# Kernel optimization log

Measured on AMD Instinct MI355X. Metric: run time of the kernel, lower is better.

## Reference

```python
import jax, jax.numpy as jnp
import numpy as np
import math

B, T, D = 2, 2048, 2048
N_HEADS, N_KV_HEADS = 16, 4
HEAD_DIM = D // N_HEADS          # 128
N_GROUPS = N_HEADS // N_KV_HEADS # 4


def setup_inputs() -> dict:
    key = jax.random.key(0)
    k1, k2, k3, k4, k5 = jax.random.split(key, 5)
    x = jax.random.normal(k1, (B, T, D), dtype=jnp.float32)
    # RoPE table: [T, head_dim//2, 2] = (cos, sin)
    inv_freq = 1.0 / (10000.0 ** (np.arange(0, HEAD_DIM, 2, dtype=np.float32) / HEAD_DIM))
    ang = np.arange(T, dtype=np.float32)[:, None] * inv_freq[None, :]  # [T, hd/2]
    rope = jnp.asarray(np.stack([np.cos(ang), np.sin(ang)], axis=-1), dtype=jnp.float32)
    s = 0.02
    wq = s * jax.random.normal(k2, (N_HEADS * HEAD_DIM, D), dtype=jnp.float32)
    wk = s * jax.random.normal(k3, (N_KV_HEADS * HEAD_DIM, D), dtype=jnp.float32)
    wv = s * jax.random.normal(k4, (N_KV_HEADS * HEAD_DIM, D), dtype=jnp.float32)
    wo = s * jax.random.normal(k5, (D, D), dtype=jnp.float32)
    return {"x": x, "rope": rope, "wq": wq, "wk": wk, "wv": wv, "wo": wo}


def apply_rope(t, rope):
    # t: [B, H, T, hd]; rope: [T, hd/2, 2]
    d = t.shape[-1]
    t1, t2 = t[..., : d // 2], t[..., d // 2 :]
    cos = rope[..., 0][None, None]  # [1,1,T,hd/2]
    sin = rope[..., 1][None, None]
    return jnp.concatenate([t1 * cos - t2 * sin, t1 * sin + t2 * cos], axis=-1)


def reference(x, rope, wq, wk, wv, wo):
    b, t, c = x.shape
    q = (x @ wq.T).reshape(b, t, N_HEADS, HEAD_DIM).transpose(0, 2, 1, 3)
    k = (x @ wk.T).reshape(b, t, N_KV_HEADS, HEAD_DIM).transpose(0, 2, 1, 3)
    v = (x @ wv.T).reshape(b, t, N_KV_HEADS, HEAD_DIM).transpose(0, 2, 1, 3)
    q = apply_rope(q, rope)
    k = apply_rope(k, rope)
    k = jnp.repeat(k, N_GROUPS, axis=1)  # [B, H, T, hd]
    v = jnp.repeat(v, N_GROUPS, axis=1)
    scale = 1.0 / math.sqrt(HEAD_DIM)
    scores = jnp.einsum("bhqd,bhkd->bhqk", q, k) * scale
    causal = jnp.tril(jnp.ones((t, t), dtype=bool))
    scores = jnp.where(causal[None, None], scores, jnp.finfo(scores.dtype).min)
    attn = jax.nn.softmax(scores, axis=-1)
    y = jnp.einsum("bhqk,bhkd->bhqd", attn, v)
    y = y.transpose(0, 2, 1, 3).reshape(b, t, c)
    return y @ wo.T
```

## Files before the change

### kernel.cpp

```cpp
#include <hip/hip_runtime.h>

typedef unsigned short u16;
typedef float   f32x4  __attribute__((ext_vector_type(4)));
typedef short   short8 __attribute__((ext_vector_type(8)));
typedef __bf16  bf16x8 __attribute__((ext_vector_type(8)));
typedef float   float4v __attribute__((ext_vector_type(4)));
typedef unsigned short u16x4 __attribute__((ext_vector_type(4)));

static __device__ __forceinline__ u16 f2b(float f) {
  return __builtin_bit_cast(u16, (__bf16)f);
}
static __device__ __forceinline__ float b2f(u16 h) {
  union { unsigned u; float f; } v; v.u = ((unsigned)h) << 16;
  return v.f;
}
static __device__ __forceinline__ f32x4 mfma_bf16(short8 a, short8 b, f32x4 c) {
  return __builtin_amdgcn_mfma_f32_16x16x32_bf16(
      __builtin_bit_cast(bf16x8, a), __builtin_bit_cast(bf16x8, b), c, 0, 0, 0);
}
static __device__ __forceinline__ void gload_lds16(const u16* g, u16* l) {
  __builtin_amdgcn_global_load_lds(
      (const __attribute__((address_space(1))) unsigned int*)g,
      (__attribute__((address_space(3))) unsigned int*)l, 16, 0, 0);
}

#define BB 2
#define TT 2048
#define DD 2048
#define NH 16
#define NKVH 4
#define HD 128
#define MM (BB * TT)
#define QSTR 3072
#define QSCALE 0.08838834764831845f

#define N4_X   ((MM * DD) / 4)
#define N4_WQ  ((DD * DD) / 4)
#define N4_WKV ((NKVH * HD * DD) / 4)
#define N4_WO  ((DD * DD) / 4)
#define N4_TOT (N4_X + N4_WQ + 2 * N4_WKV + N4_WO)

__global__ __launch_bounds__(256) void cvt_all(const float* __restrict__ x,
                                               const float* __restrict__ wq,
                                               const float* __restrict__ wk,
                                               const float* __restrict__ wv,
                                               const float* __restrict__ wo,
                                               u16* __restrict__ xb,
                                               u16* __restrict__ wqkvb,
                                               u16* __restrict__ wob) {
  int stride = gridDim.x * blockDim.x;
  for (int i = blockIdx.x * blockDim.x + threadIdx.x; i < N4_TOT; i += stride) {
    const float4v* src;
    u16x4* dst;
    int off;
    if (i < N4_X) {
      src = (const float4v*)x; dst = (u16x4*)xb; off = i;
    } else if (i < N4_X + N4_WQ) {
      src = (const float4v*)wq; dst = (u16x4*)wqkvb; off = i - N4_X;
    } else if (i < N4_X + N4_WQ + N4_WKV) {
      src = (const float4v*)wk; dst = (u16x4*)wqkvb + N4_WQ; off = i - (N4_X + N4_WQ);
    } else if (i < N4_X + N4_WQ + 2 * N4_WKV) {
      src = (const float4v*)wv; dst = (u16x4*)wqkvb + N4_WQ + N4_WKV;
      off = i - (N4_X + N4_WQ + N4_WKV);
    } else {
      src = (const float4v*)wo; dst = (u16x4*)wob; off = i - (N4_X + N4_WQ + 2 * N4_WKV);
    }
    float4v v = src[off];
    u16x4 o;
    o[0] = f2b(v[0]); o[1] = f2b(v[1]); o[2] = f2b(v[2]); o[3] = f2b(v[3]);
    dst[off] = o;
  }
}

__global__ __launch_bounds__(256) void rope_k(u16* __restrict__ K,
                                              const float* __restrict__ rope) {
  int idx = blockIdx.x * 256 + threadIdx.x;
  int i  = idx & 63;
  int h  = (idx >> 6) & (NKVH - 1);
  int bt = idx >> 8;
  int t  = bt & (TT - 1);
  size_t base = (size_t)bt * QSTR + h * HD + i;
  float x1 = b2f(K[base]);
  float x2 = b2f(K[base + 64]);
  float c = rope[t * 128 + 2 * i];
  float s = rope[t * 128 + 2 * i + 1];
  K[base]      = f2b(x1 * c - x2 * s);
  K[base + 64] = f2b(x1 * s + x2 * c);
}

__global__ __launch_bounds__(512, 2) void gemm_qkv(const u16* __restrict__ A,
                                                   const u16* __restrict__ W,
                                                   u16* __restrict__ C,
                                                   int M, int N, int K) {
  __shared__ __align__(16) u16 As[2][2][128 * 64];
  __shared__ __align__(16) u16 Ws[2][2][128 * 64];

  const int tid = threadIdx.x, lane = tid & 63, wid = tid >> 6;
  const int wm = wid >> 2, wn = wid & 3;
  const int l15 = lane & 15, lh = lane >> 4;

  const int nwg = gridDim.x * gridDim.y;
  const int lin = blockIdx.y * gridDim.x + blockIdx.x;
  const int swz = (lin & 7) * (nwg >> 3) + (lin >> 3);
  const int brow = (swz / gridDim.x) * 256, bcol = (swz % gridDim.x) * 256;

  const int srp = wid * 8 + (lane >> 3);
  const int gsw = ((lane & 7) ^ (lane >> 3)) << 3;
  const u16* sa[2][2];
  const u16* sw[2][2];
#pragma unroll
  for (int mh = 0; mh < 2; ++mh)
#pragma unroll
    for (int i = 0; i < 2; ++i) {
      sa[mh][i] = A + (size_t)(brow + mh * 128 + i * 64 + srp) * K + gsw;
      sw[mh][i] = W + (size_t)(bcol + mh * 128 + i * 64 + srp) * K + gsw;
    }

  f32x4 acc[8][4];
#pragma unroll
  for (int mi = 0; mi < 8; ++mi)
#pragma unroll
    for (int ni = 0; ni < 4; ++ni) acc[mi][ni] = (f32x4)0.0f;

  const int nk = K >> 6;

  auto issue = [&](int t, int p) {
#pragma unroll
    for (int mh = 0; mh < 2; ++mh)
#pragma unroll
      for (int i = 0; i < 2; ++i) {
        gload_lds16(sa[mh][i] + t * 64, &As[p][mh][i * 4096 + wid * 512]);
        gload_lds16(sw[mh][i] + t * 64, &Ws[p][mh][i * 4096 + wid * 512]);
      }
  };

  issue(0, 0);
  for (int t = 0; t < nk; ++t) {
    const int p = t & 1;
    if (t + 1 < nk) {
      issue(t + 1, p ^ 1);
      asm volatile("s_waitcnt vmcnt(8)" ::: "memory");
    } else {
      asm volatile("s_waitcnt vmcnt(0)" ::: "memory");
    }
    __builtin_amdgcn_sched_barrier(0);
    __builtin_amdgcn_s_barrier();
    __builtin_amdgcn_sched_barrier(0);

    const u16* Ab = &As[p][wm][0];
    const u16* Wb = &Ws[p][wn >> 1][0];
    const int wrow = (wn & 1) * 64;

    short8 af[4][2], bf[2][2];
#pragma unroll
    for (int mi = 0; mi < 4; ++mi)
#pragma unroll
      for (int ks = 0; ks < 2; ++ks) {
        int rh = mi * 16 + l15;
        af[mi][ks] = *(const short8*)&Ab[rh * 64 + (((ks * 4 + lh) ^ (rh & 7)) << 3)];
      }
#pragma unroll
    for (int ni = 0; ni < 2; ++ni)
#pragma unroll
      for (int ks = 0; ks < 2; ++ks) {
        int rh = wrow + ni * 16 + l15;
        bf[ni][ks] = *(const short8*)&Wb[rh * 64 + (((ks * 4 + lh) ^ (rh & 7)) << 3)];
      }
    __builtin_amdgcn_s_setprio(1);
#pragma unroll
    for (int mi = 0; mi < 4; ++mi)
#pragma unroll
      for (int ni = 0; ni < 2; ++ni)
#pragma unroll
        for (int ks = 0; ks < 2; ++ks)
          acc[mi][ni] = mfma_bf16(af[mi][ks], bf[ni][ks], acc[mi][ni]);
    __builtin_amdgcn_s_setprio(0);
    __builtin_amdgcn_s_barrier();
#pragma unroll
    for (int ni = 0; ni < 2; ++ni)
#pragma unroll
      for (int ks = 0; ks < 2; ++ks) {
        int rh = wrow + (2 + ni) * 16 + l15;
        bf[ni][ks] = *(const short8*)&Wb[rh * 64 + (((ks * 4 + lh) ^ (rh & 7)) << 3)];
      }
    __builtin_amdgcn_s_setprio(1);
#pragma unroll
    for (int mi = 0; mi < 4; ++mi)
#pragma unroll
      for (int ni = 0; ni < 2; ++ni)
#pragma unroll
        for (int ks = 0; ks < 2; ++ks)
          acc[mi][2 + ni] = mfma_bf16(af[mi][ks], bf[ni][ks], acc[mi][2 + ni]);
    __builtin_amdgcn_s_setprio(0);
    __builtin_amdgcn_s_barrier();
#pragma unroll
    for (int mi = 0; mi < 4; ++mi)
#pragma unroll
      for (int ks = 0; ks < 2; ++ks) {
        int rh = (4 + mi) * 16 + l15;
        af[mi][ks] = *(const short8*)&Ab[rh * 64 + (((ks * 4 + lh) ^ (rh & 7)) << 3)];
      }
    __builtin_amdgcn_s_setprio(1);
#pragma unroll
    for (int mi = 0; mi < 4; ++mi)
#pragma unroll
      for (int ni = 0; ni < 2; ++ni)
#pragma unroll
        for (int ks = 0; ks < 2; ++ks)
          acc[4 + mi][2 + ni] = mfma_bf16(af[mi][ks], bf[ni][ks], acc[4 + mi][2 + ni]);
    __builtin_amdgcn_s_setprio(0);
    __builtin_amdgcn_s_barrier();
#pragma unroll
    for (int ni = 0; ni < 2; ++ni)
#pragma unroll
      for (int ks = 0; ks < 2; ++ks) {
        int rh = wrow + ni * 16 + l15;
        bf[ni][ks] = *(const short8*)&Wb[rh * 64 + (((ks * 4 + lh) ^ (rh & 7)) << 3)];
      }
    __builtin_amdgcn_s_setprio(1);
#pragma unroll
    for (int mi = 0; mi < 4; ++mi)
#pragma unroll
      for (int ni = 0; ni < 2; ++ni)
#pragma unroll
        for (int ks = 0; ks < 2; ++ks)
          acc[4 + mi][ni] = mfma_bf16(af[mi][ks], bf[ni][ks], acc[4 + mi][ni]);
    __builtin_amdgcn_s_setprio(0);

    asm volatile("s_waitcnt lgkmcnt(0)" ::: "memory");
    __builtin_amdgcn_sched_barrier(0);
    __builtin_amdgcn_s_barrier();
    __builtin_amdgcn_sched_barrier(0);
  }

#pragma unroll
  for (int mi = 0; mi < 8; ++mi)
#pragma unroll
    for (int ni = 0; ni < 4; ++ni)
#pragma unroll
      for (int j = 0; j < 4; ++j) {
        int row = brow + wm * 128 + mi * 16 + lh * 4 + j;
        int col = bcol + wn * 64 + ni * 16 + l15;
        C[(size_t)row * N + col] = f2b(acc[mi][ni][j]);
      }
}

__global__ __launch_bounds__(512, 2) void gemm_wo(const u16* __restrict__ A,
                                                  const u16* __restrict__ W,
                                                  float* __restrict__ C,
                                                  int M, int N, int K) {
  __shared__ __align__(16) u16 As[2][2][128 * 64];
  __shared__ __align__(16) u16 Ws[2][128 * 64];

  const int tid = threadIdx.x, lane = tid & 63, wid = tid >> 6;
  const int wm = wid >> 2, wn = wid & 3;
  const int l15 = lane & 15, lh = lane >> 4;

  const int nwg = gridDim.x * gridDim.y;
  const int lin = blockIdx.y * gridDim.x + blockIdx.x;
  const int swz = (lin & 7) * (nwg >> 3) + (lin >> 3);
  const int brow = (swz / gridDim.x) * 256, bcol = (swz % gridDim.x) * 128;

  const int srp = wid * 8 + (lane >> 3);
  const int gsw = ((lane & 7) ^ (lane >> 3)) << 3;
  const u16* sa[2][2];
  const u16* sw2[2];
#pragma unroll
  for (int mh = 0; mh < 2; ++mh)
#pragma unroll
    for (int i = 0; i < 2; ++i)
      sa[mh][i] = A + (size_t)(brow + mh * 128 + i * 64 + srp) * K + gsw;
#pragma unroll
  for (int i = 0; i < 2; ++i)
    sw2[i] = W + (size_t)(bcol + i * 64 + srp) * K + gsw;

  f32x4 acc[8][2];
#pragma unroll
  for (int mi = 0; mi < 8; ++mi)
#pragma unroll
    for (int ni = 0; ni < 2; ++ni) acc[mi][ni] = (f32x4)0.0f;

  const int nk = K >> 6;

  auto issue = [&](int t, int p) {
#pragma unroll
    for (int mh = 0; mh < 2; ++mh)
#pragma unroll
      for (int i = 0; i < 2; ++i)
        gload_lds16(sa[mh][i] + t * 64, &As[p][mh][i * 4096 + wid * 512]);
#pragma unroll
    for (int i = 0; i < 2; ++i)
      gload_lds16(sw2[i] + t * 64, &Ws[p][i * 4096 + wid * 512]);
  };

  issue(0, 0);
  for (int t = 0; t < nk; ++t) {
    const int p = t & 1;
    if (t + 1 < nk) {
      issue(t + 1, p ^ 1);
      asm volatile("s_waitcnt vmcnt(6)" ::: "memory");
    } else {
      asm volatile("s_waitcnt vmcnt(0)" ::: "memory");
    }
    __builtin_amdgcn_sched_barrier(0);
    __builtin_amdgcn_s_barrier();
    __builtin_amdgcn_sched_barrier(0);

    const u16* Ab = &As[p][wm][0];
    const u16* Wb = &Ws[p][0];

    short8 af[4][2], bf[2][2];
#pragma unroll
    for (int ni = 0; ni < 2; ++ni)
#pragma unroll
      for (int ks = 0; ks < 2; ++ks) {
        int rh = wn * 32 + ni * 16 + l15;
        bf[ni][ks] = *(const short8*)&Wb[rh * 64 + (((ks * 4 + lh) ^ (rh & 7)) << 3)];
      }
#pragma unroll
    for (int mi = 0; mi < 4; ++mi)
#pragma unroll
      for (int ks = 0; ks < 2; ++ks) {
        int rh = mi * 16 + l15;
        af[mi][ks] = *(const short8*)&Ab[rh * 64 + (((ks * 4 + lh) ^ (rh & 7)) << 3)];
      }
    __builtin_amdgcn_s_setprio(1);
#pragma unroll
    for (int mi = 0; mi < 4; ++mi)
#pragma unroll
      for (int ni = 0; ni < 2; ++ni)
#pragma unroll
        for (int ks = 0; ks < 2; ++ks)
          acc[mi][ni] = mfma_bf16(af[mi][ks], bf[ni][ks], acc[mi][ni]);
    __builtin_amdgcn_s_setprio(0);
    __builtin_amdgcn_s_barrier();
#pragma unroll
    for (int mi = 0; mi < 4; ++mi)
#pragma unroll
      for (int ks = 0; ks < 2; ++ks) {
        int rh = (4 + mi) * 16 + l15;
        af[mi][ks] = *(const short8*)&Ab[rh * 64 + (((ks * 4 + lh) ^ (rh & 7)) << 3)];
      }
    __builtin_amdgcn_s_setprio(1);
#pragma unroll
    for (int mi = 0; mi < 4; ++mi)
#pragma unroll
      for (int ni = 0; ni < 2; ++ni)
#pragma unroll
        for (int ks = 0; ks < 2; ++ks)
          acc[4 + mi][ni] = mfma_bf16(af[mi][ks], bf[ni][ks], acc[4 + mi][ni]);
    __builtin_amdgcn_s_setprio(0);

    asm volatile("s_waitcnt lgkmcnt(0)" ::: "memory");
    __builtin_amdgcn_sched_barrier(0);
    __builtin_amdgcn_s_barrier();
    __builtin_amdgcn_sched_barrier(0);
  }

#pragma unroll
  for (int mi = 0; mi < 8; ++mi)
#pragma unroll
    for (int ni = 0; ni < 2; ++ni)
#pragma unroll
      for (int j = 0; j < 4; ++j) {
        int row = brow + wm * 128 + mi * 16 + lh * 4 + j;
        int col = bcol + wn * 32 + ni * 16 + l15;
        C[(size_t)row * N + col] = acc[mi][ni][j];
      }
}

#define QBLK 128
#define KVBLK 128

static __device__ __forceinline__ void attn_tile(
    const short8* qa, f32x4* o, float& l, float& m,
    int qrow0, int kv0,
    const u16* Ks, const unsigned* Vt32, u16* myP,
    int l15, int lh) {
  if (kv0 > qrow0 + 15) return;

  f32x4 st[4];
#pragma unroll
  for (int nt = 0; nt < 4; ++nt) st[nt] = (f32x4)0.0f;
  __builtin_amdgcn_s_setprio(1);
#pragma unroll
  for (int nt = 0; nt < 4; ++nt) {
    const u16* krow = &Ks[(nt * 16 + l15) * 136 + (lh << 3)];
#pragma unroll
    for (int kk = 0; kk < 4; ++kk) {
      short8 kb = *(const short8*)(krow + kk * 32);
      st[nt] = mfma_bf16(kb, qa[kk], st[nt]);
    }
  }
  __builtin_amdgcn_s_setprio(0);

  const int kvq = kv0 + lh * 4 - qrow0 - l15;
#pragma unroll
  for (int nt = 0; nt < 4; ++nt)
#pragma unroll
    for (int j = 0; j < 4; ++j)
      if (kvq + nt * 16 + j > 0) st[nt][j] = -1e30f;

  float mt = st[0][0];
#pragma unroll
  for (int nt = 0; nt < 4; ++nt)
#pragma unroll
    for (int j = 0; j < 4; ++j) mt = fmaxf(mt, st[nt][j]);
  mt = fmaxf(mt, __shfl_xor(mt, 16));
  mt = fmaxf(mt, __shfl_xor(mt, 32));

  if (!__all(mt - m <= 8.0f)) {
    float mn = fmaxf(m, mt);
    float a = __expf(m - mn);
    m = mn;
    l *= a;
    float aj[4];
#pragma unroll
    for (int j = 0; j < 4; ++j) aj[j] = __shfl(a, lh * 4 + j);
#pragma unroll
    for (int n = 0; n < 8; ++n)
#pragma unroll
      for (int j = 0; j < 4; ++j) o[n][j] *= aj[j];
  }

  f32x4 p[4];
  float ps = 0.0f;
#pragma unroll
  for (int nt = 0; nt < 4; ++nt) {
#pragma unroll
    for (int j = 0; j < 4; ++j) p[nt][j] = __expf(st[nt][j] - m);
    ps += (p[nt][0] + p[nt][1]) + (p[nt][2] + p[nt][3]);
  }
  l += ps;

  unsigned* P32 = (unsigned*)myP;
  const int pb = l15 * 36 + lh * 2;
#pragma unroll
  for (int nt = 0; nt < 4; ++nt)
#pragma unroll
    for (int jj = 0; jj < 2; ++jj)
      P32[pb + nt * 8 + jj] =
          (unsigned)f2b(p[nt][2 * jj]) | ((unsigned)f2b(p[nt][2 * jj + 1]) << 16);

  __builtin_amdgcn_s_setprio(1);
#pragma unroll
  for (int c = 0; c < 2; ++c) {
    short8 pa = *(const short8*)&myP[l15 * 72 + c * 32 + (lh << 3)];
#pragma unroll
    for (int nt2 = 0; nt2 < 8; ++nt2) {
      int d = nt2 * 16 + l15;
      int byteoff = (d * 144 + (c * 32 + lh * 8) * 2) ^ (((d >> 3) & 7) << 4);
      short8 vb = *(const short8*)((const char*)Vt32 + byteoff);
      o[nt2] = mfma_bf16(pa, vb, o[nt2]);
    }
  }
  __builtin_amdgcn_s_setprio(0);
}

__global__ __launch_bounds__(512) void attn_kernel(const u16* __restrict__ QKV,
                                                   const float* __restrict__ rope,
                                                   u16* __restrict__ Y) {
  __shared__ __align__(16) u16 Ks[2][64 * 136];
  __shared__ __align__(16) unsigned Vt32[2][128 * 36];
  __shared__ __align__(16) u16 Ps[8][16 * 72];

  const int tid = threadIdx.x, lane = tid & 63, wid = tid >> 6;
  const int l15 = lane & 15, lh = lane >> 4;
  const int bid = blockIdx.x;
  const int qpair = bid & 7;
  const int h = (bid >> 3) & 15;
  const int b = bid >> 7;
  const int kvh = h >> 2;
  const int qtA = qpair, qtB = 15 - qpair;
  const int rowA = qtA * QBLK + wid * 16;
  const int rowB = qtB * QBLK + wid * 16;

  const u16* Kb_ = QKV + (size_t)b * TT * QSTR + DD + kvh * HD;
  const u16* Vb_ = Kb_ + NKVH * HD;

  short8 qaA[4], qaB[4];
  {
    const u16* qA = QKV + (size_t)(b * TT + rowA + l15) * QSTR + h * HD + (lh << 3);
    const u16* qB = QKV + (size_t)(b * TT + rowB + l15) * QSTR + h * HD + (lh << 3);
#pragma unroll
    for (int kk = 0; kk < 4; ++kk) {
      qaA[kk] = *(const short8*)(qA + kk * 32);
      qaB[kk] = *(const short8*)(qB + kk * 32);
    }
  }
  {
    const float* rpA = rope + (size_t)(rowA + l15) * 128;
    const float* rpB = rope + (size_t)(rowB + l15) * 128;
#pragma unroll
    for (int kk = 0; kk < 2; ++kk)
#pragma unroll
      for (int e = 0; e < 8; ++e) {
        const int i2 = 2 * (kk * 32 + (lh << 3) + e);
        float c = rpA[i2], s = rpA[i2 + 1];
        float x1 = b2f((u16)qaA[kk][e]), x2 = b2f((u16)qaA[kk + 2][e]);
        qaA[kk][e]     = (short)f2b(QSCALE * (x1 * c - x2 * s));
        qaA[kk + 2][e] = (short)f2b(QSCALE * (x1 * s + x2 * c));
        float cb = rpB[i2], sb = rpB[i2 + 1];
        float y1 = b2f((u16)qaB[kk][e]), y2 = b2f((u16)qaB[kk + 2][e]);
        qaB[kk][e]     = (short)f2b(QSCALE * (y1 * cb - y2 * sb));
        qaB[kk + 2][e] = (short)f2b(QSCALE * (y1 * sb + y2 * cb));
      }
  }

  f32x4 oA[8], oB[8];
  float lA = 0.0f, lB = 0.0f;
  float mA = -1e30f, mB = -1e30f;
#pragma unroll
  for (int n = 0; n < 8; ++n) { oA[n] = (f32x4)0.0f; oB[n] = (f32x4)0.0f; }

  const int kvend = (qtB + 1) * QBLK;

  short8 kreg[4], vreg[4];
  const int srow = tid >> 4;
  const int sc8 = (tid & 15) << 3;

  auto issue = [&](int kv0) {
    kreg[0] = *(const short8*)&Kb_[(size_t)(kv0 + srow) * QSTR + sc8];
    kreg[1] = *(const short8*)&Kb_[(size_t)(kv0 + 32 + srow) * QSTR + sc8];
    kreg[2] = *(const short8*)&Kb_[(size_t)(kv0 + 64 + srow) * QSTR + sc8];
    kreg[3] = *(const short8*)&Kb_[(size_t)(kv0 + 96 + srow) * QSTR + sc8];
    vreg[0] = *(const short8*)&Vb_[(size_t)(kv0 + 2 * srow) * QSTR + sc8];
    vreg[1] = *(const short8*)&Vb_[(size_t)(kv0 + 2 * srow + 1) * QSTR + sc8];
    vreg[2] = *(const short8*)&Vb_[(size_t)(kv0 + 64 + 2 * srow) * QSTR + sc8];
    vreg[3] = *(const short8*)&Vb_[(size_t)(kv0 + 64 + 2 * srow + 1) * QSTR + sc8];
  };

  issue(0);
  for (int kv0 = 0; kv0 < kvend; kv0 += KVBLK) {
    __syncthreads();
    *(short8*)&Ks[0][srow * 136 + sc8] = kreg[0];
    *(short8*)&Ks[0][(srow + 32) * 136 + sc8] = kreg[1];
    *(short8*)&Ks[1][srow * 136 + sc8] = kreg[2];
    *(short8*)&Ks[1][(srow + 32) * 136 + sc8] = kreg[3];
#pragma unroll
    for (int e = 0; e < 8; ++e) {
      int d = sc8 + e;
      unsigned pk0 = (unsigned)(u16)vreg[0][e] | ((unsigned)(u16)vreg[1][e] << 16);
      unsigned pk1 = (unsigned)(u16)vreg[2][e] | ((unsigned)(u16)vreg[3][e] << 16);
      int byteoff = (d * 144 + 4 * srow) ^ (((d >> 3) & 7) << 4);
      *(unsigned*)((char*)&Vt32[0][0] + byteoff) = pk0;
      *(unsigned*)((char*)&Vt32[1][0] + byteoff) = pk1;
    }
    __syncthreads();
    if (kv0 + KVBLK < kvend) issue(kv0 + KVBLK);

    attn_tile(qaA, oA, lA, mA, rowA, kv0,      &Ks[0][0], &Vt32[0][0], &Ps[wid][0], l15, lh);
    attn_tile(qaA, oA, lA, mA, rowA, kv0 + 64, &Ks[1][0], &Vt32[1][0], &Ps[wid][0], l15, lh);
    attn_tile(qaB, oB, lB, mB, rowB, kv0,      &Ks[0][0], &Vt32[0][0], &Ps[wid][0], l15, lh);
    attn_tile(qaB, oB, lB, mB, rowB, kv0 + 64, &Ks[1][0], &Vt32[1][0], &Ps[wid][0], l15, lh);
  }

  lA += __shfl_xor(lA, 16); lA += __shfl_xor(lA, 32);
  lB += __shfl_xor(lB, 16); lB += __shfl_xor(lB, 32);
  f32x4 invA, invB;
#pragma unroll
  for (int j = 0; j < 4; ++j) {
    invA[j] = __builtin_amdgcn_rcpf(__shfl(lA, lh * 4 + j));
    invB[j] = __builtin_amdgcn_rcpf(__shfl(lB, lh * 4 + j));
  }
#pragma unroll
  for (int nt = 0; nt < 8; ++nt)
#pragma unroll
    for (int j = 0; j < 4; ++j) {
      Y[(size_t)(b * TT + rowA + lh * 4 + j) * DD + h * HD + nt * 16 + l15] =
          f2b(oA[nt][j] * invA[j]);
      Y[(size_t)(b * TT + rowB + lh * 4 + j) * DD + h * HD + nt * 16 + l15] =
          f2b(oB[nt][j] * invB[j]);
    }
}

extern "C" void kernel_launch(void* const* d_in, const int* in_sizes, int n_in,
                              void* d_out, int out_size, void* d_ws, size_t ws_size,
                              hipStream_t stream) {
  const float* x    = (const float*)d_in[0];
  const float* rope = (const float*)d_in[1];
  const float* wq   = (const float*)d_in[2];
  const float* wk   = (const float*)d_in[3];
  const float* wv   = (const float*)d_in[4];
  const float* wo   = (const float*)d_in[5];
  float* out = (float*)d_out;

  char* ws = (char*)d_ws;
  u16* xb    = (u16*)ws; ws += (size_t)MM * DD * 2;
  u16* wqkvb = (u16*)ws; ws += (size_t)QSTR * DD * 2;
  u16* wob   = (u16*)ws; ws += (size_t)DD * DD * 2;
  u16* QKVb  = (u16*)ws; ws += (size_t)MM * QSTR * 2;
  u16* Yb    = (u16*)ws;

  cvt_all<<<2048, 256, 0, stream>>>(x, wq, wk, wv, wo, xb, wqkvb, wob);

  gemm_qkv<<<dim3(QSTR / 256, MM / 256), 512, 0, stream>>>(xb, wqkvb, QKVb, MM, QSTR, DD);

  rope_k<<<(MM * NKVH * 64) / 256, 256, 0, stream>>>(QKVb + DD, rope);

  attn_kernel<<<BB * NH * (TT / QBLK / 2), 512, 0, stream>>>(QKVb, rope, Yb);

  gemm_wo<<<dim3(DD / 128, MM / 256), 512, 0, stream>>>(Yb, wob, out, MM, DD, DD);
}
```

Before: 212.3 us.

## Retile QKV GEMM to 256x192 output blocks for better CU fill

Changes the QKV projection GEMM tile from 256x256 to 256x192. Each wave now loads all three 16-wide B fragments once per k-step and runs two MFMA phases instead of four, and the LDS staging for W shrinks to 192 rows. With QSTR=3072 and M=4096 this gives 16x16=256 workgroups instead of 12x16=192, to fill the 256 CUs of MI355X in a single wave. In exchange it drops the 2-blocks-per-CU launch bound hint and lowers arithmetic intensity per tile.

```diff
diff --git a/kernel.cpp b/kernel.cpp
--- a/kernel.cpp
+++ b/kernel.cpp
@@ -88,12 +88,12 @@
   K[base + 64] = f2b(x1 * s + x2 * c);
 }
 
-__global__ __launch_bounds__(512, 2) void gemm_qkv(const u16* __restrict__ A,
-                                                   const u16* __restrict__ W,
-                                                   u16* __restrict__ C,
-                                                   int M, int N, int K) {
+__global__ __launch_bounds__(512) void gemm_qkv(const u16* __restrict__ A,
+                                                const u16* __restrict__ W,
+                                                u16* __restrict__ C,
+                                                int M, int N, int K) {
   __shared__ __align__(16) u16 As[2][2][128 * 64];
-  __shared__ __align__(16) u16 Ws[2][2][128 * 64];
+  __shared__ __align__(16) u16 Ws[2][192 * 64];
 
   const int tid = threadIdx.x, lane = tid & 63, wid = tid >> 6;
   const int wm = wid >> 2, wn = wid & 3;
@@ -102,25 +102,26 @@
   const int nwg = gridDim.x * gridDim.y;
   const int lin = blockIdx.y * gridDim.x + blockIdx.x;
   const int swz = (lin & 7) * (nwg >> 3) + (lin >> 3);
-  const int brow = (swz / gridDim.x) * 256, bcol = (swz % gridDim.x) * 256;
+  const int brow = (swz / gridDim.x) * 256, bcol = (swz % gridDim.x) * 192;
 
   const int srp = wid * 8 + (lane >> 3);
   const int gsw = ((lane & 7) ^ (lane >> 3)) << 3;
   const u16* sa[2][2];
-  const u16* sw[2][2];
+  const u16* sw3[3];
 #pragma unroll
   for (int mh = 0; mh < 2; ++mh)
 #pragma unroll
-    for (int i = 0; i < 2; ++i) {
+    for (int i = 0; i < 2; ++i)
       sa[mh][i] = A + (size_t)(brow + mh * 128 + i * 64 + srp) * K + gsw;
-      sw[mh][i] = W + (size_t)(bcol + mh * 128 + i * 64 + srp) * K + gsw;
-    }
-
-  f32x4 acc[8][4];
+#pragma unroll
+  for (int i = 0; i < 3; ++i)
+    sw3[i] = W + (size_t)(bcol + i * 64 + srp) * K + gsw;
+
+  f32x4 acc[8][3];
 #pragma unroll
   for (int mi = 0; mi < 8; ++mi)
 #pragma unroll
-    for (int ni = 0; ni < 4; ++ni) acc[mi][ni] = (f32x4)0.0f;
+    for (int ni = 0; ni < 3; ++ni) acc[mi][ni] = (f32x4)0.0f;
 
   const int nk = K >> 6;
 
@@ -128,10 +129,11 @@
 #pragma unroll
     for (int mh = 0; mh < 2; ++mh)
 #pragma unroll
-      for (int i = 0; i < 2; ++i) {
+      for (int i = 0; i < 2; ++i)
         gload_lds16(sa[mh][i] + t * 64, &As[p][mh][i * 4096 + wid * 512]);
-        gload_lds16(sw[mh][i] + t * 64, &Ws[p][mh][i * 4096 + wid * 512]);
-      }
+#pragma unroll
+    for (int i = 0; i < 3; ++i)
+      gload_lds16(sw3[i] + t * 64, &Ws[p][i * 4096 + wid * 512]);
   };
 
   issue(0, 0);
@@ -139,7 +141,7 @@
     const int p = t & 1;
     if (t + 1 < nk) {
       issue(t + 1, p ^ 1);
-      asm volatile("s_waitcnt vmcnt(8)" ::: "memory");
+      asm volatile("s_waitcnt vmcnt(7)" ::: "memory");
     } else {
       asm volatile("s_waitcnt vmcnt(0)" ::: "memory");
     }
@@ -148,10 +150,16 @@
     __builtin_amdgcn_sched_barrier(0);
 
     const u16* Ab = &As[p][wm][0];
-    const u16* Wb = &Ws[p][wn >> 1][0];
-    const int wrow = (wn & 1) * 64;
-
-    short8 af[4][2], bf[2][2];
+    const u16* Wb = &Ws[p][0];
+
+    short8 af[4][2], bf[3][2];
+#pragma unroll
+    for (int ni = 0; ni < 3; ++ni)
+#pragma unroll
+      for (int ks = 0; ks < 2; ++ks) {
+        int rh = wn * 48 + ni * 16 + l15;
+        bf[ni][ks] = *(const short8*)&Wb[rh * 64 + (((ks * 4 + lh) ^ (rh & 7)) << 3)];
+      }
 #pragma unroll
     for (int mi = 0; mi < 4; ++mi)
 #pragma unroll
@@ -159,41 +167,17 @@
         int rh = mi * 16 + l15;
         af[mi][ks] = *(const short8*)&Ab[rh * 64 + (((ks * 4 + lh) ^ (rh & 7)) << 3)];
       }
-#pragma unroll
-    for (int ni = 0; ni < 2; ++ni)
-#pragma unroll
-      for (int ks = 0; ks < 2; ++ks) {
-        int rh = wrow + ni * 16 + l15;
-        bf[ni][ks] = *(const short8*)&Wb[rh * 64 + (((ks * 4 + lh) ^ (rh & 7)) << 3)];
-      }
     __builtin_amdgcn_s_setprio(1);
 #pragma unroll
     for (int mi = 0; mi < 4; ++mi)
 #pragma unroll
-      for (int ni = 0; ni < 2; ++ni)
+      for (int ni = 0; ni < 3; ++ni)
 #pragma unroll
         for (int ks = 0; ks < 2; ++ks)
           acc[mi][ni] = mfma_bf16(af[mi][ks], bf[ni][ks], acc[mi][ni]);
     __builtin_amdgcn_s_setprio(0);
     __builtin_amdgcn_s_barrier();
 #pragma unroll
-    for (int ni = 0; ni < 2; ++ni)
-#pragma unroll
-      for (int ks = 0; ks < 2; ++ks) {
-        int rh = wrow + (2 + ni) * 16 + l15;
-        bf[ni][ks] = *(const short8*)&Wb[rh * 64 + (((ks * 4 + lh) ^ (rh & 7)) << 3)];
-      }
-    __builtin_amdgcn_s_setprio(1);
-#pragma unroll
-    for (int mi = 0; mi < 4; ++mi)
-#pragma unroll
-      for (int ni = 0; ni < 2; ++ni)
-#pragma unroll
-        for (int ks = 0; ks < 2; ++ks)
-          acc[mi][2 + ni] = mfma_bf16(af[mi][ks], bf[ni][ks], acc[mi][2 + ni]);
-    __builtin_amdgcn_s_setprio(0);
-    __builtin_amdgcn_s_barrier();
-#pragma unroll
     for (int mi = 0; mi < 4; ++mi)
 #pragma unroll
       for (int ks = 0; ks < 2; ++ks) {
@@ -204,24 +188,7 @@
 #pragma unroll
     for (int mi = 0; mi < 4; ++mi)
 #pragma unroll
-      for (int ni = 0; ni < 2; ++ni)
-#pragma unroll
-        for (int ks = 0; ks < 2; ++ks)
-          acc[4 + mi][2 + ni] = mfma_bf16(af[mi][ks], bf[ni][ks], acc[4 + mi][2 + ni]);
-    __builtin_amdgcn_s_setprio(0);
-    __builtin_amdgcn_s_barrier();
-#pragma unroll
-    for (int ni = 0; ni < 2; ++ni)
-#pragma unroll
-      for (int ks = 0; ks < 2; ++ks) {
-        int rh = wrow + ni * 16 + l15;
-        bf[ni][ks] = *(const short8*)&Wb[rh * 64 + (((ks * 4 + lh) ^ (rh & 7)) << 3)];
-      }
-    __builtin_amdgcn_s_setprio(1);
-#pragma unroll
-    for (int mi = 0; mi < 4; ++mi)
-#pragma unroll
-      for (int ni = 0; ni < 2; ++ni)
+      for (int ni = 0; ni < 3; ++ni)
 #pragma unroll
         for (int ks = 0; ks < 2; ++ks)
           acc[4 + mi][ni] = mfma_bf16(af[mi][ks], bf[ni][ks], acc[4 + mi][ni]);
@@ -236,11 +203,11 @@
 #pragma unroll
   for (int mi = 0; mi < 8; ++mi)
 #pragma unroll
-    for (int ni = 0; ni < 4; ++ni)
+    for (int ni = 0; ni < 3; ++ni)
 #pragma unroll
       for (int j = 0; j < 4; ++j) {
         int row = brow + wm * 128 + mi * 16 + lh * 4 + j;
-        int col = bcol + wn * 64 + ni * 16 + l15;
+        int col = bcol + wn * 48 + ni * 16 + l15;
         C[(size_t)row * N + col] = f2b(acc[mi][ni][j]);
       }
 }
@@ -594,7 +561,7 @@
 
   cvt_all<<<2048, 256, 0, stream>>>(x, wq, wk, wv, wo, xb, wqkvb, wob);
 
-  gemm_qkv<<<dim3(QSTR / 256, MM / 256), 512, 0, stream>>>(xb, wqkvb, QKVb, MM, QSTR, DD);
+  gemm_qkv<<<dim3(QSTR / 192, MM / 256), 512, 0, stream>>>(xb, wqkvb, QKVb, MM, QSTR, DD);
 
   rope_k<<<(MM * NKVH * 64) / 256, 256, 0, stream>>>(QKVb + DD, rope);
 
```

Result: faster. 200.1 us (-5.8%).
